# Optimization experiments

Hardware: AMD Instinct MI355X
Metric: run time of the kernel (lower is better)

Reference implementation:

```python
import jax, jax.numpy as jnp
import numpy as np

BN_EPS = 1e-5
# regular 3x3 kernel grid offsets: row0 = dy, row1 = dx, kernel positions in row-major order
REG = jnp.array([[-1, -1, -1, 0, 0, 0, 1, 1, 1],
                 [-1,  0,  1, -1, 0, 1, -1, 0, 1]], dtype=jnp.float32)


def conv3x3(x, w, b):
    y = jax.lax.conv_general_dilated(x, w, window_strides=(1, 1),
                                     padding=((1, 1), (1, 1)),
                                     dimension_numbers=('NCHW', 'OIHW', 'NCHW'))
    return y + b[None, :, None, None]


def deform_conv3x3(x, dy, dx, w):
    # x: [N,C,H,W]; dy,dx: [N,9,H,W] per-kernel-tap offsets; w: [O,C,3,3]
    N, C, H, W = x.shape
    K = 9
    ky = jnp.repeat(jnp.arange(3), 3)   # [0,0,0,1,1,1,2,2,2]
    kx = jnp.tile(jnp.arange(3), 3)     # [0,1,2,0,1,2,0,1,2]
    # sampling positions: p = p_out - pad + k*dilation + offset (stride=1, pad=dil=1)
    py = dy + (jnp.arange(H) - 1)[None, None, :, None] + ky[None, :, None, None].astype(x.dtype)
    px = dx + (jnp.arange(W) - 1)[None, None, None, :] + kx[None, :, None, None].astype(x.dtype)
    y0 = jnp.floor(py)
    x0 = jnp.floor(px)
    wy = py - y0  # bilinear weights
    wx = px - x0
    y0i = y0.astype(jnp.int32)
    x0i = x0.astype(jnp.int32)
    nidx = jnp.arange(N)[:, None, None, None]

    def gather(yi, xi):
        valid = ((yi >= 0) & (yi < H) & (xi >= 0) & (xi < W)).astype(x.dtype)
        v = x[nidx, :, jnp.clip(yi, 0, H - 1), jnp.clip(xi, 0, W - 1)]  # [N,K,H,W,C]
        return v * valid[..., None]

    sampled = (gather(y0i,     x0i)     * ((1 - wy) * (1 - wx))[..., None]
             + gather(y0i,     x0i + 1) * ((1 - wy) * wx)[..., None]
             + gather(y0i + 1, x0i)     * (wy * (1 - wx))[..., None]
             + gather(y0i + 1, x0i + 1) * (wy * wx)[..., None])  # [N,K,H,W,C]
    O = w.shape[0]
    return jnp.einsum('nkhwc,ock->nohw', sampled, w.reshape(O, C, K))


def setup_inputs() -> dict:
    key = jax.random.key(0)
    ks = jax.random.split(key, 12)
    N, C, H, W = 2, 256, 96, 96
    O = 256
    sc = 1.0 / np.sqrt(C * 9)
    return {
        'x': jax.random.normal(ks[0], (N, C, H, W), jnp.float32),
        'mask_attention': jax.random.normal(ks[1], (N, C, H, W), jnp.float32),
        'w_tm': jax.random.normal(ks[2], (4, C, 3, 3), jnp.float32) * sc,
        'b_tm': jax.random.normal(ks[3], (4,), jnp.float32) * 0.01,
        'w_tr': jax.random.normal(ks[4], (2, C, 3, 3), jnp.float32) * sc,
        'b_tr': jax.random.normal(ks[5], (2,), jnp.float32) * 0.01,
        'w_deform': jax.random.normal(ks[6], (O, C, 3, 3), jnp.float32) * sc,
        'bn_gamma': jnp.ones((O,), jnp.float32),
        'bn_beta': jnp.zeros((O,), jnp.float32),
        'bn_mean': jax.random.normal(ks[7], (O,), jnp.float32) * 0.01,
        'bn_var': jax.random.uniform(ks[8], (O,), jnp.float32, 0.5, 1.5),
    }


def reference(x, mask_attention, w_tm, b_tm, w_tr, b_tr, w_deform,
              bn_gamma, bn_beta, bn_mean, bn_var):
    # mask_attention is overwritten by x in the original forward; ignored.
    N, C, H, W = x.shape
    tm = conv3x3(x, w_tm, b_tm)                       # [N,4,H,W]
    T = tm.transpose(0, 2, 3, 1).reshape(N, H, W, 2, 2)
    off = jnp.einsum('nhwij,jk->nhwik', T, REG) - REG  # [N,H,W,2,9], (T-I)@REG
    tr = conv3x3(x, w_tr, b_tr)                        # [N,2,H,W]
    off = off + tr.transpose(0, 2, 3, 1)[..., None]    # broadcast translation to all 9 taps
    dy = off[..., 0, :].transpose(0, 3, 1, 2)          # [N,9,H,W]
    dx = off[..., 1, :].transpose(0, 3, 1, 2)
    out = deform_conv3x3(x, dy, dx, w_deform)          # [N,O,H,W]
    inv = jax.lax.rsqrt(bn_var + BN_EPS)
    out = (out - bn_mean[None, :, None, None]) * (inv * bn_gamma)[None, :, None, None] \
          + bn_beta[None, :, None, None]
    return jax.nn.relu(out + x)
```

## Files before the change

### kernel.cpp

```cpp
#include <hip/hip_runtime.h>
#include <stdint.h>

#define H_ 96
#define W_ 96
#define C_ 256
#define O_ 256
#define N_ 2
#define HW_ (H_*W_)
#define M_ (N_*HW_)
#define GK 2304

typedef _Float16 f16x8 __attribute__((ext_vector_type(8)));
typedef _Float16 f16x2 __attribute__((ext_vector_type(2)));
typedef float f32x4 __attribute__((ext_vector_type(4)));
typedef unsigned short us4 __attribute__((ext_vector_type(4)));
typedef unsigned short us8 __attribute__((ext_vector_type(8)));

__device__ __forceinline__ unsigned short f2h(float f) {
  union { _Float16 h; unsigned short u; } v;
  v.h = (_Float16)f;
  return v.u;
}

__global__ __launch_bounds__(256) void k_pre(const float* __restrict__ x,
                                             const float* __restrict__ w_df,
                                             const float* __restrict__ w_tm,
                                             const float* __restrict__ w_tr,
                                             unsigned short* __restrict__ xt,
                                             unsigned short* __restrict__ wfrag,
                                             unsigned short* __restrict__ w6p) {
  const int b = blockIdx.x;
  const int tid = threadIdx.x;
  if (b < 576) {
    __shared__ unsigned short tile[64][130];
    const int pt = b % 144;
    const int ch = (b / 144) & 1;
    const int n  = b / 288;
    const int p0 = pt * 64, c0 = ch * 128;
    const float* xp = x + (size_t)n * C_ * HW_;
    unsigned short* xtp = xt + (size_t)n * C_ * HW_;
    const int tx = tid & 15, ty = tid >> 4;
#pragma unroll
    for (int pass = 0; pass < 8; pass++) {
      const int c = pass * 16 + ty;
      const f32x4 v = *(const f32x4*)(xp + (size_t)(c0 + c) * HW_ + p0 + tx * 4);
#pragma unroll
      for (int i = 0; i < 4; i++) tile[tx * 4 + i][c] = f2h(v[i]);
    }
    __syncthreads();
    const int l32 = tid & 31, pr = tid >> 5;
#pragma unroll
    for (int pass = 0; pass < 8; pass++) {
      const int p = pass * 8 + pr;
      us4 v;
#pragma unroll
      for (int i = 0; i < 4; i++) v[i] = tile[p][l32 * 4 + i];
      *(us4*)(xtp + (size_t)(p0 + p) * C_ + c0 + l32 * 4) = v;
    }
  } else if (b < 864) {
    const int base = (b - 576) * 2048 + tid * 8;
    const int l  = (base >> 3) & 63;
    const int g  = (base >> 9) & 15;
    const int ks = (base >> 13) & 7;
    const int t  = base >> 16;
    const int o  = g * 16 + (l & 15);
    const int c  = ks * 32 + (l >> 4) * 8;
    us8 res;
#pragma unroll
    for (int j = 0; j < 8; j++) res[j] = f2h(w_df[(size_t)(o * 256 + c + j) * 9 + t]);
    *(us8*)(wfrag + base) = res;
  } else {
    int idx = (b - 864) * 256 + tid;
    int t = idx >> 12;
    int r = idx & 4095;
    int j = r >> 8;
    int c = r & 255;
    float v = 0.f;
    if (j < 4) v = w_tm[(size_t)(j * C_ + c) * 9 + t];
    else if (j < 6) v = w_tr[(size_t)((j - 4) * C_ + c) * 9 + t];
    w6p[idx] = f2h(v);
  }
}

__global__ __launch_bounds__(512, 2) void k_fused(const unsigned short* __restrict__ xt,
                                                  const unsigned short* __restrict__ Wfrag,
                                                  const unsigned short* __restrict__ w6p,
                                                  const float* __restrict__ b_tm,
                                                  const float* __restrict__ b_tr,
                                                  const float* __restrict__ xres,
                                                  const float* __restrict__ gamma,
                                                  const float* __restrict__ beta,
                                                  const float* __restrict__ mean,
                                                  const float* __restrict__ var,
                                                  float* __restrict__ out) {
  __shared__ unsigned short As[2][32 * 256] __attribute__((aligned(16)));
  __shared__ float sred[8][16][8];
  __shared__ float coords_s[32][9][2];
  const int tid = threadIdx.x;
  const int wave = tid >> 6, lane = tid & 63;
  const int row = lane & 15, quad = lane >> 4;
  const int bm = (blockIdx.x & 7) * 72 + (blockIdx.x >> 3);
  const int m0 = bm * 32;
  const int n = m0 / HW_;
  const int sr = tid >> 4;
  const int cg = tid & 15;

  {
    const int hw0 = m0 - n * HW_;
    const int h = hw0 / W_;
    const int w0 = hw0 - h * W_;
    const int rh = wave >> 2;
    const int cq = (wave & 3) * 64;
    f32x4 oacc = {0.f, 0.f, 0.f, 0.f};
    const f16x8 zero8 = {};
#pragma unroll
    for (int t = 0; t < 9; t++) {
      const int ty = t / 3, tx = t % 3;
      const int y = h + ty - 1;
      if (y < 0 || y >= H_) continue;
      const int xx = w0 + rh * 16 + row + tx - 1;
      const bool valid = (xx >= 0) && (xx < W_);
      const int xc = min(max(xx, 0), W_ - 1);
      const unsigned short* arow =
          xt + (size_t)((n * H_ + y) * W_ + xc) * C_ + cq + quad * 8;
      const unsigned short* brow =
          w6p + (size_t)(t * 16 + row) * C_ + cq + quad * 8;
#pragma unroll
      for (int ks = 0; ks < 2; ks++) {
        f16x8 av = *(const f16x8*)(const void*)(arow + ks * 32);
        if (!valid) av = zero8;
        f16x8 bv = *(const f16x8*)(const void*)(brow + ks * 32);
        oacc = __builtin_amdgcn_mfma_f32_16x16x32_f16(av, bv, oacc, 0, 0, 0);
      }
    }
    if (row < 6) {
#pragma unroll
      for (int r = 0; r < 4; r++) sred[wave][quad * 4 + r][row] = oacc[r];
    }
  }
  __syncthreads();
  if (wave < 2 && lane < 16) {
    const int rg = wave * 16 + lane;
    const int hwm = m0 + rg - n * HW_;
    const int h = hwm / W_, w = hwm - h * W_;
    float a[6];
#pragma unroll
    for (int j = 0; j < 6; j++)
      a[j] = sred[wave * 4 + 0][lane][j] + sred[wave * 4 + 1][lane][j] +
             sred[wave * 4 + 2][lane][j] + sred[wave * 4 + 3][lane][j];
    const float tm0 = a[0] + b_tm[0];
    const float tm1 = a[1] + b_tm[1];
    const float tm2 = a[2] + b_tm[2];
    const float tm3 = a[3] + b_tm[3];
    const float tr0 = a[4] + b_tr[0];
    const float tr1 = a[5] + b_tr[1];
#pragma unroll
    for (int t = 0; t < 9; t++) {
      const float ry = (float)(t / 3) - 1.f;
      const float rx = (float)(t % 3) - 1.f;
      coords_s[rg][t][0] = (float)h + tr0 + tm0 * ry + tm1 * rx;
      coords_s[rg][t][1] = (float)w + tr1 + tm2 * ry + tm3 * rx;
    }
  }
  __syncthreads();

  f32x4 acc0[2] = {}, acc1[2] = {};
  f16x2 cwh0, cwh1, cwh2, cwh3;
  int cb[4];
  us8 u0[4], u1[4];

#define PREP1(TAP)                                                             \
  {                                                                            \
    const float py = coords_s[sr][TAP][0];                                     \
    const float px = coords_s[sr][TAP][1];                                     \
    const float fy = floorf(py), fx = floorf(px);                              \
    const float wy = py - fy, wx = px - fx;                                    \
    const int y0 = (int)fy, x0 = (int)fx;                                      \
    const int y1 = y0 + 1, x1 = x0 + 1;                                        \
    const float vy0 = (y0 >= 0 && y0 < H_) ? 1.f : 0.f;                        \
    const float vy1 = (y1 >= 0 && y1 < H_) ? 1.f : 0.f;                        \
    const float vx0 = (x0 >= 0 && x0 < W_) ? 1.f : 0.f;                        \
    const float vx1 = (x1 >= 0 && x1 < W_) ? 1.f : 0.f;                        \
    const float c0f = (1.f - wy) * (1.f - wx) * vy0 * vx0;                     \
    const float c1f = (1.f - wy) * wx * vy0 * vx1;                             \
    const float c2f = wy * (1.f - wx) * vy1 * vx0;                             \
    const float c3f = wy * wx * vy1 * vx1;                                     \
    const _Float16 h0 = (_Float16)c0f, h1 = (_Float16)c1f;                     \
    const _Float16 h2 = (_Float16)c2f, h3 = (_Float16)c3f;                     \
    cwh0 = (f16x2){h0, h0}; cwh1 = (f16x2){h1, h1};                            \
    cwh2 = (f16x2){h2, h2}; cwh3 = (f16x2){h3, h3};                            \
    const int cy0 = min(max(y0, 0), H_ - 1), cy1 = min(max(y1, 0), H_ - 1);    \
    const int cx0 = min(max(x0, 0), W_ - 1), cx1 = min(max(x1, 0), W_ - 1);    \
    cb[0] = ((n * H_ + cy0) * W_ + cx0) * C_;                                  \
    cb[1] = ((n * H_ + cy0) * W_ + cx1) * C_;                                  \
    cb[2] = ((n * H_ + cy1) * W_ + cx0) * C_;                                  \
    cb[3] = ((n * H_ + cy1) * W_ + cx1) * C_;                                  \
  }

#define LOADC1()                                                               \
  {                                                                            \
    const int cc = cg * 16;                                                    \
    u0[0] = *(const us8*)(xt + cb[0] + cc); u1[0] = *(const us8*)(xt + cb[0] + cc + 8); \
    u0[1] = *(const us8*)(xt + cb[1] + cc); u1[1] = *(const us8*)(xt + cb[1] + cc + 8); \
    u0[2] = *(const us8*)(xt + cb[2] + cc); u1[2] = *(const us8*)(xt + cb[2] + cc + 8); \
    u0[3] = *(const us8*)(xt + cb[3] + cc); u1[3] = *(const us8*)(xt + cb[3] + cc + 8); \
  }

#define LERP8V(DST, U)                                                         \
  {                                                                            \
    const f16x2* p0 = (const f16x2*)&U[0];                                     \
    const f16x2* p1 = (const f16x2*)&U[1];                                     \
    const f16x2* p2 = (const f16x2*)&U[2];                                     \
    const f16x2* p3 = (const f16x2*)&U[3];                                     \
    f16x2* d = (f16x2*)&DST;                                                   \
    _Pragma("unroll")                                                          \
    for (int p = 0; p < 4; p++) {                                              \
      f16x2 r = p0[p] * cwh0;                                                  \
      r = p1[p] * cwh1 + r;                                                    \
      r = p2[p] * cwh2 + r;                                                    \
      r = p3[p] * cwh3 + r;                                                    \
      d[p] = r;                                                                \
    }                                                                          \
  }

#define KSTEP(KS, Bx, By)                                                      \
  {                                                                            \
    const int q = (KS) * 4 + quad;                                             \
    const int slt = (q & 24) | ((q ^ row) & 7);                                \
    const f16x8 av0 = *(const f16x8*)(const void*)&asb[row * 256 + slt * 8];   \
    const f16x8 av1 = *(const f16x8*)(const void*)&asb[(row + 16) * 256 + slt * 8]; \
    f16x8 nx, ny;                                                              \
    if ((KS) < 6) {                                                            \
      const unsigned short* wfn = wfTap + (size_t)((KS) + 2) * 8192;           \
      nx = *(const f16x8*)(const void*)(wfn);                                  \
      ny = *(const f16x8*)(const void*)(wfn + 512);                            \
    }                                                                          \
    acc0[0] = __builtin_amdgcn_mfma_f32_16x16x32_f16(av0, Bx, acc0[0], 0, 0, 0); \
    acc0[1] = __builtin_amdgcn_mfma_f32_16x16x32_f16(av0, By, acc0[1], 0, 0, 0); \
    acc1[0] = __builtin_amdgcn_mfma_f32_16x16x32_f16(av1, Bx, acc1[0], 0, 0, 0); \
    acc1[1] = __builtin_amdgcn_mfma_f32_16x16x32_f16(av1, By, acc1[1], 0, 0, 0); \
    if ((KS) < 6) { Bx = nx; By = ny; }                                        \
  }

  PREP1(0);
  LOADC1();

  for (int tap = 0; tap < 9; tap++) {
    unsigned short* __restrict__ asb = As[tap & 1];
    const unsigned short* wfTap =
        Wfrag + (size_t)(tap * 8) * 8192 + wave * 1024 + lane * 8;

    f16x8 B0 = *(const f16x8*)(const void*)(wfTap);
    f16x8 B1 = *(const f16x8*)(const void*)(wfTap + 512);
    f16x8 B2 = *(const f16x8*)(const void*)(wfTap + 8192);
    f16x8 B3 = *(const f16x8*)(const void*)(wfTap + 8704);
    __builtin_amdgcn_sched_barrier(0);

    {
      const int q0 = cg * 2, q1 = cg * 2 + 1;
      const int s0 = (q0 & 24) | ((q0 ^ sr) & 7);
      const int s1 = (q1 & 24) | ((q1 ^ sr) & 7);
      us8 r0, r1;
      LERP8V(r0, u0);
      LERP8V(r1, u1);
      *(us8*)(void*)&asb[sr * 256 + s0 * 8] = r0;
      *(us8*)(void*)&asb[sr * 256 + s1 * 8] = r1;
    }

    __syncthreads();

    if (tap < 8) {
      PREP1(tap + 1);
      LOADC1();
    }
    __builtin_amdgcn_sched_barrier(0);

    KSTEP(0, B0, B1)
    KSTEP(1, B2, B3)
    KSTEP(2, B0, B1)
    KSTEP(3, B2, B3)
    KSTEP(4, B0, B1)
    KSTEP(5, B2, B3)
    KSTEP(6, B0, B1)
    KSTEP(7, B2, B3)
  }

  const int hwb = m0 - n * HW_ + quad * 4;
#pragma unroll
  for (int ot = 0; ot < 2; ot++) {
    const int o = wave * 32 + ot * 16 + row;
    const float sc = rsqrtf(var[o] + 1e-5f) * gamma[o];
    const float bi = beta[o] - mean[o] * sc;
    const size_t ob0 = (size_t)(n * O_ + o) * HW_ + hwb;
    f32x4 rv = *(const f32x4*)(xres + ob0);
    f32x4 ov;
#pragma unroll
    for (int r = 0; r < 4; r++) ov[r] = fmaxf(acc0[ot][r] * sc + bi + rv[r], 0.f);
    *(f32x4*)(out + ob0) = ov;
    const size_t ob1 = ob0 + 16;
    rv = *(const f32x4*)(xres + ob1);
#pragma unroll
    for (int r = 0; r < 4; r++) ov[r] = fmaxf(acc1[ot][r] * sc + bi + rv[r], 0.f);
    *(f32x4*)(out + ob1) = ov;
  }
}

extern "C" void kernel_launch(void* const* d_in, const int* in_sizes, int n_in,
                              void* d_out, int out_size, void* d_ws, size_t ws_size,
                              hipStream_t stream) {
  const float* x     = (const float*)d_in[0];
  const float* w_tm  = (const float*)d_in[2];
  const float* b_tm  = (const float*)d_in[3];
  const float* w_tr  = (const float*)d_in[4];
  const float* b_tr  = (const float*)d_in[5];
  const float* w_df  = (const float*)d_in[6];
  const float* gamma = (const float*)d_in[7];
  const float* beta  = (const float*)d_in[8];
  const float* mean  = (const float*)d_in[9];
  const float* var   = (const float*)d_in[10];
  float* out = (float*)d_out;

  char* ws = (char*)d_ws;
  unsigned short* xt    = (unsigned short*)(ws);
  unsigned short* wfrag = (unsigned short*)(ws + 9437184);
  unsigned short* w6p   = (unsigned short*)(ws + 9437184 + 1179648);

  k_pre<<<1008, 256, 0, stream>>>(x, w_df, w_tm, w_tr, xt, wfrag, w6p);
  k_fused<<<576, 512, 0, stream>>>(xt, wfrag, w6p, b_tm, b_tr, x,
                                   gamma, beta, mean, var, out);
}
```

Before: 182.9 us.

## Gather all nine taps into LDS before a single fully unrolled MFMA loop

Replaces the per-tap double-buffered gather/MFMA loop with a two-phase scheme. All nine bilinear-sampled tap tiles are first written into a 9-slot LDS buffer using ping-pong register prefetch, followed by one barrier and a fully unrolled 72-step MFMA loop with register-prefetched A and B fragments. This removes eight block barriers and decouples gather latency from the MFMA stream. It raises LDS use to roughly 150KB per block, which limits residency to one block per CU and removes the cross-block overlap of gathers and math.

New measurement: 176.0 us. -3.8%, faster.

```diff
diff --git a/kernel.cpp b/kernel.cpp
--- a/kernel.cpp
+++ b/kernel.cpp
@@ -20,6 +20,10 @@
   union { _Float16 h; unsigned short u; } v;
   v.h = (_Float16)f;
   return v.u;
+}
+__device__ __forceinline__ f16x2 hpair(float f) {
+  const _Float16 h = (_Float16)f;
+  return (f16x2){h, h};
 }
 
 __global__ __launch_bounds__(256) void k_pre(const float* __restrict__ x,
@@ -93,7 +97,7 @@
                                                   const float* __restrict__ mean,
                                                   const float* __restrict__ var,
                                                   float* __restrict__ out) {
-  __shared__ unsigned short As[2][32 * 256] __attribute__((aligned(16)));
+  __shared__ unsigned short As9[9][32 * 256] __attribute__((aligned(16)));
   __shared__ float sred[8][16][8];
   __shared__ float coords_s[32][9][2];
   const int tid = threadIdx.x;
@@ -164,12 +168,10 @@
   }
   __syncthreads();
 
-  f32x4 acc0[2] = {}, acc1[2] = {};
-  f16x2 cwh0, cwh1, cwh2, cwh3;
-  int cb[4];
-  us8 u0[4], u1[4];
-
-#define PREP1(TAP)                                                             \
+  f16x2 cwA0, cwA1, cwA2, cwA3, cwB0, cwB1, cwB2, cwB3;
+  us8 uA0[4], uA1[4], uB0[4], uB1[4];
+
+#define PL(TAP, S)                                                             \
   {                                                                            \
     const float py = coords_s[sr][TAP][0];                                     \
     const float px = coords_s[sr][TAP][1];                                     \
@@ -181,108 +183,117 @@
     const float vy1 = (y1 >= 0 && y1 < H_) ? 1.f : 0.f;                        \
     const float vx0 = (x0 >= 0 && x0 < W_) ? 1.f : 0.f;                        \
     const float vx1 = (x1 >= 0 && x1 < W_) ? 1.f : 0.f;                        \
-    const float c0f = (1.f - wy) * (1.f - wx) * vy0 * vx0;                     \
-    const float c1f = (1.f - wy) * wx * vy0 * vx1;                             \
-    const float c2f = wy * (1.f - wx) * vy1 * vx0;                             \
-    const float c3f = wy * wx * vy1 * vx1;                                     \
-    const _Float16 h0 = (_Float16)c0f, h1 = (_Float16)c1f;                     \
-    const _Float16 h2 = (_Float16)c2f, h3 = (_Float16)c3f;                     \
-    cwh0 = (f16x2){h0, h0}; cwh1 = (f16x2){h1, h1};                            \
-    cwh2 = (f16x2){h2, h2}; cwh3 = (f16x2){h3, h3};                            \
+    cw##S##0 = hpair((1.f - wy) * (1.f - wx) * vy0 * vx0);                     \
+    cw##S##1 = hpair((1.f - wy) * wx * vy0 * vx1);                             \
+    cw##S##2 = hpair(wy * (1.f - wx) * vy1 * vx0);                             \
+    cw##S##3 = hpair(wy * wx * vy1 * vx1);                                     \
     const int cy0 = min(max(y0, 0), H_ - 1), cy1 = min(max(y1, 0), H_ - 1);    \
     const int cx0 = min(max(x0, 0), W_ - 1), cx1 = min(max(x1, 0), W_ - 1);    \
-    cb[0] = ((n * H_ + cy0) * W_ + cx0) * C_;                                  \
-    cb[1] = ((n * H_ + cy0) * W_ + cx1) * C_;                                  \
-    cb[2] = ((n * H_ + cy1) * W_ + cx0) * C_;                                  \
-    cb[3] = ((n * H_ + cy1) * W_ + cx1) * C_;                                  \
-  }
-
-#define LOADC1()                                                               \
+    const int b0 = ((n * H_ + cy0) * W_ + cx0) * C_ + cg * 16;                 \
+    const int b1 = ((n * H_ + cy0) * W_ + cx1) * C_ + cg * 16;                 \
+    const int b2 = ((n * H_ + cy1) * W_ + cx0) * C_ + cg * 16;                 \
+    const int b3 = ((n * H_ + cy1) * W_ + cx1) * C_ + cg * 16;                 \
+    u##S##0[0] = *(const us8*)(xt + b0); u##S##1[0] = *(const us8*)(xt + b0 + 8); \
+    u##S##0[1] = *(const us8*)(xt + b1); u##S##1[1] = *(const us8*)(xt + b1 + 8); \
+    u##S##0[2] = *(const us8*)(xt + b2); u##S##1[2] = *(const us8*)(xt + b2 + 8); \
+    u##S##0[3] = *(const us8*)(xt + b3); u##S##1[3] = *(const us8*)(xt + b3 + 8); \
+  }
+
+#define LERPS(DST, U, C0, C1, C2, C3)                                          \
   {                                                                            \
-    const int cc = cg * 16;                                                    \
-    u0[0] = *(const us8*)(xt + cb[0] + cc); u1[0] = *(const us8*)(xt + cb[0] + cc + 8); \
-    u0[1] = *(const us8*)(xt + cb[1] + cc); u1[1] = *(const us8*)(xt + cb[1] + cc + 8); \
-    u0[2] = *(const us8*)(xt + cb[2] + cc); u1[2] = *(const us8*)(xt + cb[2] + cc + 8); \
-    u0[3] = *(const us8*)(xt + cb[3] + cc); u1[3] = *(const us8*)(xt + cb[3] + cc + 8); \
-  }
-
-#define LERP8V(DST, U)                                                         \
-  {                                                                            \
-    const f16x2* p0 = (const f16x2*)&U[0];                                     \
-    const f16x2* p1 = (const f16x2*)&U[1];                                     \
-    const f16x2* p2 = (const f16x2*)&U[2];                                     \
-    const f16x2* p3 = (const f16x2*)&U[3];                                     \
+    const f16x2* q0 = (const f16x2*)&U[0];                                     \
+    const f16x2* q1 = (const f16x2*)&U[1];                                     \
+    const f16x2* q2 = (const f16x2*)&U[2];                                     \
+    const f16x2* q3 = (const f16x2*)&U[3];                                     \
     f16x2* d = (f16x2*)&DST;                                                   \
     _Pragma("unroll")                                                          \
     for (int p = 0; p < 4; p++) {                                              \
-      f16x2 r = p0[p] * cwh0;                                                  \
-      r = p1[p] * cwh1 + r;                                                    \
-      r = p2[p] * cwh2 + r;                                                    \
-      r = p3[p] * cwh3 + r;                                                    \
+      f16x2 r = q0[p] * C0;                                                    \
+      r = q1[p] * C1 + r;                                                      \
+      r = q2[p] * C2 + r;                                                      \
+      r = q3[p] * C3 + r;                                                      \
       d[p] = r;                                                                \
     }                                                                          \
   }
 
-#define KSTEP(KS, Bx, By)                                                      \
+#define LS(TAP, S)                                                             \
   {                                                                            \
-    const int q = (KS) * 4 + quad;                                             \
-    const int slt = (q & 24) | ((q ^ row) & 7);                                \
-    const f16x8 av0 = *(const f16x8*)(const void*)&asb[row * 256 + slt * 8];   \
-    const f16x8 av1 = *(const f16x8*)(const void*)&asb[(row + 16) * 256 + slt * 8]; \
-    f16x8 nx, ny;                                                              \
-    if ((KS) < 6) {                                                            \
-      const unsigned short* wfn = wfTap + (size_t)((KS) + 2) * 8192;           \
+    unsigned short* asb = &As9[TAP][0];                                        \
+    const int q0i = cg * 2, q1i = cg * 2 + 1;                                  \
+    const int s0 = (q0i & 24) | ((q0i ^ sr) & 7);                              \
+    const int s1 = (q1i & 24) | ((q1i ^ sr) & 7);                              \
+    us8 r0, r1;                                                                \
+    LERPS(r0, u##S##0, cw##S##0, cw##S##1, cw##S##2, cw##S##3);                \
+    LERPS(r1, u##S##1, cw##S##0, cw##S##1, cw##S##2, cw##S##3);                \
+    *(us8*)(void*)&asb[sr * 256 + s0 * 8] = r0;                                \
+    *(us8*)(void*)&asb[sr * 256 + s1 * 8] = r1;                                \
+  }
+
+  PL(0, A);
+  PL(1, B);
+  __builtin_amdgcn_sched_barrier(0);
+  LS(0, A); PL(2, A); __builtin_amdgcn_sched_barrier(0);
+  LS(1, B); PL(3, B); __builtin_amdgcn_sched_barrier(0);
+  LS(2, A); PL(4, A); __builtin_amdgcn_sched_barrier(0);
+  LS(3, B); PL(5, B); __builtin_amdgcn_sched_barrier(0);
+  LS(4, A); PL(6, A); __builtin_amdgcn_sched_barrier(0);
+  LS(5, B); PL(7, B); __builtin_amdgcn_sched_barrier(0);
+  LS(6, A); PL(8, A); __builtin_amdgcn_sched_barrier(0);
+  LS(7, B);
+  LS(8, A);
+
+  __syncthreads();
+
+  f32x4 acc0[2] = {}, acc1[2] = {};
+  const unsigned short* wfW = Wfrag + wave * 1024 + lane * 8;
+
+  f16x8 P0 = *(const f16x8*)(const void*)(wfW + (size_t)0 * 8192);
+  f16x8 P1 = *(const f16x8*)(const void*)(wfW + (size_t)0 * 8192 + 512);
+  f16x8 P2 = *(const f16x8*)(const void*)(wfW + (size_t)1 * 8192);
+  f16x8 P3 = *(const f16x8*)(const void*)(wfW + (size_t)1 * 8192 + 512);
+  f16x8 P4 = *(const f16x8*)(const void*)(wfW + (size_t)2 * 8192);
+  f16x8 P5 = *(const f16x8*)(const void*)(wfW + (size_t)2 * 8192 + 512);
+  f16x8 P6 = *(const f16x8*)(const void*)(wfW + (size_t)3 * 8192);
+  f16x8 P7 = *(const f16x8*)(const void*)(wfW + (size_t)3 * 8192 + 512);
+
+  f16x8 avc0, avc1;
+  {
+    const int q = quad;
+    const int sl = (q & 24) | ((q ^ row) & 7);
+    avc0 = *(const f16x8*)(const void*)&As9[0][row * 256 + sl * 8];
+    avc1 = *(const f16x8*)(const void*)&As9[0][(row + 16) * 256 + sl * 8];
+  }
+
+#define GS(KK, BX, BY)                                                         \
+  {                                                                            \
+    f16x8 nx, ny, an0, an1;                                                    \
+    if ((KK) < 71) {                                                           \
+      const int qn = (((KK) + 1) & 7) * 4 + quad;                              \
+      const int sln = (qn & 24) | ((qn ^ row) & 7);                            \
+      const unsigned short* ab = &As9[((KK) + 1) >> 3][0];                     \
+      an0 = *(const f16x8*)(const void*)&ab[row * 256 + sln * 8];              \
+      an1 = *(const f16x8*)(const void*)&ab[(row + 16) * 256 + sln * 8];       \
+    }                                                                          \
+    if ((KK) < 68) {                                                           \
+      const unsigned short* wfn = wfW + (size_t)((KK) + 4) * 8192;             \
       nx = *(const f16x8*)(const void*)(wfn);                                  \
       ny = *(const f16x8*)(const void*)(wfn + 512);                            \
     }                                                                          \
-    acc0[0] = __builtin_amdgcn_mfma_f32_16x16x32_f16(av0, Bx, acc0[0], 0, 0, 0); \
-    acc0[1] = __builtin_amdgcn_mfma_f32_16x16x32_f16(av0, By, acc0[1], 0, 0, 0); \
-    acc1[0] = __builtin_amdgcn_mfma_f32_16x16x32_f16(av1, Bx, acc1[0], 0, 0, 0); \
-    acc1[1] = __builtin_amdgcn_mfma_f32_16x16x32_f16(av1, By, acc1[1], 0, 0, 0); \
-    if ((KS) < 6) { Bx = nx; By = ny; }                                        \
-  }
-
-  PREP1(0);
-  LOADC1();
-
-  for (int tap = 0; tap < 9; tap++) {
-    unsigned short* __restrict__ asb = As[tap & 1];
-    const unsigned short* wfTap =
-        Wfrag + (size_t)(tap * 8) * 8192 + wave * 1024 + lane * 8;
-
-    f16x8 B0 = *(const f16x8*)(const void*)(wfTap);
-    f16x8 B1 = *(const f16x8*)(const void*)(wfTap + 512);
-    f16x8 B2 = *(const f16x8*)(const void*)(wfTap + 8192);
-    f16x8 B3 = *(const f16x8*)(const void*)(wfTap + 8704);
-    __builtin_amdgcn_sched_barrier(0);
-
-    {
-      const int q0 = cg * 2, q1 = cg * 2 + 1;
-      const int s0 = (q0 & 24) | ((q0 ^ sr) & 7);
-      const int s1 = (q1 & 24) | ((q1 ^ sr) & 7);
-      us8 r0, r1;
-      LERP8V(r0, u0);
-      LERP8V(r1, u1);
-      *(us8*)(void*)&asb[sr * 256 + s0 * 8] = r0;
-      *(us8*)(void*)&asb[sr * 256 + s1 * 8] = r1;
-    }
-
-    __syncthreads();
-
-    if (tap < 8) {
-      PREP1(tap + 1);
-      LOADC1();
-    }
-    __builtin_amdgcn_sched_barrier(0);
-
-    KSTEP(0, B0, B1)
-    KSTEP(1, B2, B3)
-    KSTEP(2, B0, B1)
-    KSTEP(3, B2, B3)
-    KSTEP(4, B0, B1)
-    KSTEP(5, B2, B3)
-    KSTEP(6, B0, B1)
-    KSTEP(7, B2, B3)
+    acc0[0] = __builtin_amdgcn_mfma_f32_16x16x32_f16(avc0, BX, acc0[0], 0, 0, 0); \
+    acc0[1] = __builtin_amdgcn_mfma_f32_16x16x32_f16(avc0, BY, acc0[1], 0, 0, 0); \
+    acc1[0] = __builtin_amdgcn_mfma_f32_16x16x32_f16(avc1, BX, acc1[0], 0, 0, 0); \
+    acc1[1] = __builtin_amdgcn_mfma_f32_16x16x32_f16(avc1, BY, acc1[1], 0, 0, 0); \
+    __builtin_amdgcn_sched_barrier(0);                                         \
+    if ((KK) < 71) { avc0 = an0; avc1 = an1; }                                 \
+    if ((KK) < 68) { BX = nx; BY = ny; }                                       \
+  }
+
+#pragma unroll
+  for (int kb = 0; kb < 72; kb += 4) {
+    GS(kb + 0, P0, P1);
+    GS(kb + 1, P2, P3);
+    GS(kb + 2, P4, P5);
+    GS(kb + 3, P6, P7);
   }
 
   const int hwb = m0 - n * HW_ + quad * 4;
```
